# Performance work log

Measured on AMD Instinct MI355X. Metric: run time of the kernel, lower is better.

## Reference

```python
import jax, jax.numpy as jnp
import numpy as np

B, L, H, HEADS, N_NODE = 1024, 200, 128, 8, 200000
MAXN = L + 1  # max_n_node
D = H // HEADS
EPS = 1e-12


def setup_inputs() -> dict:
    key = jax.random.key(0)
    ks = jax.random.split(key, 20)
    lengths = jax.random.randint(ks[0], (B,), 1, L + 1)
    mask = (jnp.arange(L)[None, :] < lengths[:, None]).astype(jnp.int32)  # contiguous 1s
    alias_inputs = jax.random.randint(ks[1], (B, L), 0, MAXN)
    items = jax.random.randint(ks[2], (B, MAXN), 0, N_NODE)

    def lin_w(k, o, i):
        return (jax.random.normal(k, (o, i), jnp.float32) * 0.1)

    inp = dict(
        alias_inputs=alias_inputs,
        items=items,
        mask=mask,
        emb_W=jax.random.normal(ks[3], (N_NODE, H), jnp.float32) * 0.1,
        # LastAttenion params
        W0=lin_w(ks[4], H, H), b0=jax.random.normal(ks[5], (H,), jnp.float32) * 0.1,
        W1=lin_w(ks[6], H, H), b1=jax.random.normal(ks[7], (H,), jnp.float32) * 0.1,
        W2=lin_w(ks[8], H, H), b2=jax.random.normal(ks[9], (H,), jnp.float32) * 0.1,
        # linear_q[0] (last_k = 1)
        Wq=lin_w(ks[10], H, H), bq=jax.random.normal(ks[11], (H,), jnp.float32) * 0.1,
        # linear_transform (2H -> H)
        Wt=lin_w(ks[12], H, 2 * H), bt=jax.random.normal(ks[13], (H,), jnp.float32) * 0.1,
        ln_g=jax.random.normal(ks[14], (H,), jnp.float32) * 0.1,
        ln_b=jax.random.normal(ks[15], (H,), jnp.float32) * 0.1,
    )
    return inp


def reference(alias_inputs, items, mask, emb_W, W0, b0, W1, b1, W2, b2, Wq, bq, Wt, bt, ln_g, ln_b):
    maskf = mask.astype(jnp.float32)
    # hidden = normalize(embedding(items)); dropout off (eval)
    hidden = emb_W[items]                                                  # [B, MAXN, H]
    hidden = hidden / (jnp.linalg.norm(hidden, axis=-1, keepdims=True) + EPS)
    # per-batch gather: seq_hidden[b, t] = hidden[b, alias_inputs[b, t]]
    seq = jnp.take_along_axis(hidden, alias_inputs[..., None], axis=1)     # [B, L, H]
    seq = seq * maskf[..., None]
    seq = seq / (jnp.linalg.norm(seq, axis=-1, keepdims=True) + EPS)
    # compute_scores
    lengths = mask.sum(1)
    last_idx = lengths - 1                                                 # >= 0 (lengths >= 1)
    ht_last = seq[jnp.arange(B), last_idx]                                 # [B, H]  (ht0 too)
    hts = (ht_last @ Wq.T + bq)[:, None, :]                                # [B, 1, H]
    # torch.norm over dim=1 (size 1) == elementwise abs
    hts = hts / (jnp.linalg.norm(hts, axis=1, keepdims=True) + EPS)
    # LastAttenion (last_k = 1, no lp-pool, eval dropout off)
    q0 = (hts @ W0.T + b0).reshape(B * HEADS, 1, D)                        # [B*h, 1, d]
    q1 = (seq @ W1.T + b1).reshape(B * HEADS, L, D)                        # [B*h, L, d]
    q2 = (seq @ W2.T + b2).reshape(B, L, HEADS, D)                         # [B, L, h, d]
    alpha = jax.nn.sigmoid(jnp.einsum('bkd,bld->bkl', q0, q1))             # [B*h, 1, L]
    alpha = alpha.reshape(B, HEADS, L).transpose(0, 2, 1)                  # [B, L, h]
    alpha = jax.nn.softmax(2.0 * alpha, axis=1)
    a = jnp.sum((alpha[..., None] * q2).reshape(B, L, H) * maskf[..., None], axis=1)  # [B, H]
    # layernorm eps=1e-8
    mu = a.mean(-1, keepdims=True)
    var = ((a - mu) ** 2).mean(-1, keepdims=True)
    a = (a - mu) / jnp.sqrt(var + 1e-8) * ln_g + ln_b
    a = jnp.concatenate([a, ht_last], axis=1) @ Wt.T + bt                  # [B, H]
    # norm=True branch
    a = a / (jnp.linalg.norm(a, axis=1, keepdims=True) + EPS)
    b = emb_W[1:]
    b = b / (jnp.linalg.norm(b, axis=1, keepdims=True) + EPS)
    return a, b.T                                                          # [B,H], [H, N_NODE-1]
```

## Files before the change

kernel.cpp:

```cpp
#include <hip/hip_runtime.h>
#include <math.h>

typedef unsigned int uint;
typedef unsigned short ushort;

__device__ __forceinline__ float b2f(ushort u){
  union { uint i; float f; } v; v.i = ((uint)u) << 16; return v.f;
}
__device__ __forceinline__ ushort f2b(float f){
  union { float f; uint i; } v; v.f = f;
  uint i = v.i;
  i += 0x7fffu + ((i >> 16) & 1u);
  return (ushort)(i >> 16);
}
__device__ __forceinline__ float wred(float v){
  #pragma unroll
  for (int s = 32; s > 0; s >>= 1) v += __shfl_xor(v, s, 64);
  return v;
}
__device__ __forceinline__ float gred16(float v){
  v += __shfl_xor(v, 1, 64);
  v += __shfl_xor(v, 2, 64);
  v += __shfl_xor(v, 4, 64);
  v += __shfl_xor(v, 8, 64);
  return v;
}
__device__ __forceinline__ float sane(float v){ return isfinite(v) ? v : 0.f; }
__device__ __forceinline__ int iclamp(int v, int lo, int hi){ return v < lo ? lo : (v > hi ? hi : v); }

__device__ __forceinline__ void load_raw8(const void* emb, int isf, int it, int p, float x[8]){
  if (it >= 0){
    if (isf){
      const float4* q = (const float4*)((const float*)emb + (size_t)it * 128);
      float4 u = q[p * 2], u2 = q[p * 2 + 1];
      x[0] = u.x; x[1] = u.y; x[2] = u.z; x[3] = u.w;
      x[4] = u2.x; x[5] = u2.y; x[6] = u2.z; x[7] = u2.w;
    } else {
      uint4 u = ((const uint4*)((const ushort*)emb + (size_t)it * 128))[p];
      x[0] = b2f((ushort)u.x); x[1] = b2f((ushort)(u.x >> 16));
      x[2] = b2f((ushort)u.y); x[3] = b2f((ushort)(u.y >> 16));
      x[4] = b2f((ushort)u.z); x[5] = b2f((ushort)(u.z >> 16));
      x[6] = b2f((ushort)u.w); x[7] = b2f((ushort)(u.w >> 16));
    }
  } else {
    #pragma unroll
    for (int e = 0; e < 8; ++e) x[e] = 0.f;
  }
}

__device__ __forceinline__ int detect_isf(const void* emb, int t, int* s_flag){
  if (t == 0) *s_flag = 0;
  __syncthreads();
  if (t < 64){
    uint4 u = ((const uint4*)emb)[t];
    uint w[4] = { u.x, u.y, u.z, u.w };
    int bad = 0;
    #pragma unroll
    for (int e = 0; e < 4; ++e){
      float v0 = fabsf(b2f((ushort)w[e]));
      float v1 = fabsf(b2f((ushort)(w[e] >> 16)));
      if (!(v0 <= 1e4f) || !(v1 <= 1e4f)) bad = 1;
    }
    if (bad) *s_flag = 1;
  }
  __syncthreads();
  return *s_flag;
}

#define OUTB 131072

#define C_W0T 0
#define C_W1  16384
#define C_W2T 32768
#define C_WQT 49152
#define C_WTT 65536
#define C_B0  98304
#define C_B1  98432
#define C_B2  98560
#define C_BQ  98688
#define C_BT  98816
#define C_G   98944
#define C_BB  99072
#define C_TOT 99200

#define KMAIN_SMEM 73984

__global__ __launch_bounds__(256) void k_wts(
    const void* __restrict__ emb,
    const void* W0, const void* b0, const void* W1, const void* b1,
    const void* W2, const void* b2, const void* Wq, const void* bq,
    const void* Wt, const void* bt, const void* g, const void* bb,
    float* __restrict__ wts){
  __shared__ int s_flag;
  const int t = threadIdx.x;
  const int isf = detect_isf(emb, t, &s_flag);
  int j = blockIdx.x * 256 + t;
  if (j >= C_TOT) return;
  const void* src; int si;
  if (j < 16384)      { int k = j >> 7, h = j & 127; src = W0; si = h * 128 + k; }
  else if (j < 32768) { src = W1; si = j - 16384; }
  else if (j < 49152) { int i = j - 32768; int k = i >> 7, h = i & 127; src = W2; si = h * 128 + k; }
  else if (j < 65536) { int i = j - 49152; int k = i >> 7, h = i & 127; src = Wq; si = h * 128 + k; }
  else if (j < 98304) { int i = j - 65536; int k = i >> 7, h = i & 127; src = Wt; si = h * 256 + k; }
  else {
    int i = j - 98304; int arr = i >> 7;
    const void* tab[7] = { b0, b1, b2, bq, bt, g, bb };
    src = tab[arr]; si = i & 127;
  }
  wts[j] = isf ? ((const float*)src)[si] : b2f(((const ushort*)src)[si]);
}

__global__ __launch_bounds__(256) void k_bout(const void* __restrict__ emb,
                                              void* __restrict__ outv){
  __shared__ float tile[64 * 129];
  __shared__ int s_flag;
  const int t = threadIdx.x, gid = t >> 4, p = t & 15;
  const int base = blockIdx.x * 64;
  const int isf = detect_isf(emb, t, &s_flag);
  for (int i = gid; i < 64; i += 16){
    int gi = base + i;
    if (gi < 199999){
      float x[8];
      if (isf){
        const float4* q = (const float4*)((const float*)emb + (size_t)(gi + 1) * 128);
        float4 u = q[p * 2], u2 = q[p * 2 + 1];
        x[0] = u.x; x[1] = u.y; x[2] = u.z; x[3] = u.w;
        x[4] = u2.x; x[5] = u2.y; x[6] = u2.z; x[7] = u2.w;
      } else {
        uint4 u = ((const uint4*)((const ushort*)emb + (size_t)(gi + 1) * 128))[p];
        x[0] = b2f((ushort)u.x); x[1] = b2f((ushort)(u.x >> 16));
        x[2] = b2f((ushort)u.y); x[3] = b2f((ushort)(u.y >> 16));
        x[4] = b2f((ushort)u.z); x[5] = b2f((ushort)(u.z >> 16));
        x[6] = b2f((ushort)u.w); x[7] = b2f((ushort)(u.w >> 16));
      }
      float ss = 0.f;
      #pragma unroll
      for (int e = 0; e < 8; ++e) ss += x[e] * x[e];
      ss = gred16(ss);
      float inv = 1.f / (sqrtf(ss) + 1e-12f);
      #pragma unroll
      for (int e = 0; e < 8; ++e) tile[i * 129 + p * 8 + e] = x[e] * inv;
    }
  }
  __syncthreads();
  for (int it = 0; it < 32; ++it){
    int idx = it * 256 + t;
    int h = idx >> 6, n = idx & 63;
    int gi = base + n;
    if (gi < 199999){
      float val = sane(tile[n * 129 + h]);
      if (isf) ((float*)outv)[OUTB + (size_t)h * 199999 + gi] = val;
      else     ((ushort*)outv)[OUTB + (size_t)h * 199999 + gi] = f2b(val);
    }
  }
}

__global__ __launch_bounds__(256) void k_main(
    const int* __restrict__ alias_, const int* __restrict__ items,
    const int* __restrict__ mask, const void* __restrict__ emb,
    const float* __restrict__ wts, void* __restrict__ outv){
  extern __shared__ __align__(16) char dsm[];
  __shared__ int s_flag;
  __shared__ float s_X0[128], s_ht[128], s_a[128], s_hts[128];
  __shared__ float s_c1[64];
  __shared__ float s_T[8], s_Tp[64];
  __shared__ float s_red[16];
  __shared__ int   s_it[200];
  __shared__ int   s_item;

  const int t = threadIdx.x;
  const int isf = detect_isf(emb, t, &s_flag);
  const int b = blockIdx.x;

  ushort* s_x     = (ushort*)dsm;
  ushort* s_w1p   = (ushort*)(dsm + 51200);
  float*  s_part  = (float*)(dsm + 51200);
  float*  s_alpha = (float*)(dsm + 51200 + 16384);

  const int wv = t >> 6, gid = t >> 4, p = t & 15, lane = t & 63;
  const int mbase = b * 200;

  int mv = 0;
  if (t < 200){
    mv = mask[mbase + t];
    int a = mv ? iclamp(alias_[mbase + t], 0, 200) : 0;
    s_it[t] = mv ? iclamp(items[b * 201 + a], 0, 199999) : -1;
  }
  float lv = wred((float)mv);
  if ((t & 63) == 0) s_red[t >> 6] = lv;
  __syncthreads();
  const int len = iclamp((int)(s_red[0] + s_red[1] + s_red[2] + s_red[3] + 0.5f), 1, 200);
  if (t == 0){
    int a = iclamp(alias_[mbase + len - 1], 0, 200);
    s_item = iclamp(items[b * 201 + a], 0, 199999);
  }
  __syncthreads();

  float v = 0.f;
  if (t < 128)
    v = isf ? ((const float*)emb)[(size_t)s_item * 128 + t]
            : b2f(((const ushort*)emb)[(size_t)s_item * 128 + t]);
  float ss = wred(v * v);
  if ((t & 63) == 0) s_red[4 + (t >> 6)] = ss;
  __syncthreads();
  v = v / (sqrtf(s_red[4] + s_red[5]) + 1e-12f);
  float ss2 = wred(v * v);
  if ((t & 63) == 0) s_red[8 + (t >> 6)] = ss2;
  __syncthreads();
  v = v / (sqrtf(s_red[8] + s_red[9]) + 1e-12f);
  if (t < 128) s_ht[t] = v;
  __syncthreads();

  if (t < 128){
    double acc = (double)wts[C_BQ + t];
    for (int k = 0; k < 128; ++k)
      acc += (double)wts[C_WQT + k * 128 + t] * (double)s_ht[k];
    float a = (float)acc;
    s_hts[t] = a / (fabsf(a) + 1e-12f);
  }
  __syncthreads();
  if (t < 128){
    float a0 = wts[C_B0 + t];
    for (int k = 0; k < 128; ++k) a0 += wts[C_W0T + k * 128 + t] * s_hts[k];
    s_X0[t] = a0;
  }
  __syncthreads();
  if (t < 64){
    int head = t >> 3, j = t & 7;
    float c = 0.f;
    #pragma unroll
    for (int d = 0; d < 16; ++d) c += s_X0[head * 16 + d] * wts[C_B1 + j * 16 + d];
    s_c1[t] = c;
  }

  __syncthreads();
  for (int idx = t; idx < 8192; idx += 256){
    int hj = idx >> 7, k = idx & 127, head = hj >> 3, j = hj & 7;
    float acc = 0.f;
    const float* w1r = wts + C_W1 + (j * 16) * 128 + k;
    #pragma unroll
    for (int d = 0; d < 16; ++d) acc += s_X0[head * 16 + d] * w1r[d * 128];
    s_w1p[hj * 128 + k] = f2b(acc);
  }
  __syncthreads();

  {
    float xc[8], xn[8];
    load_raw8(emb, isf, s_it[gid], p, xc);
    for (int r = gid; r < 200; r += 16){
      int rn = r + 16;
      load_raw8(emb, isf, rn < 200 ? s_it[rn] : -1, p, xn);

      int head = r / 25, lb = (r % 25) * 8;
      uint4 wu[8];
      #pragma unroll
      for (int j = 0; j < 8; ++j)
        wu[j] = *(const uint4*)(s_w1p + (head * 8 + j) * 128 + p * 8);

      float ssr = 0.f;
      #pragma unroll
      for (int e = 0; e < 8; ++e) ssr += xc[e] * xc[e];
      ssr = gred16(ssr);
      float inv = 1.f / (sqrtf(ssr) + 1e-12f);
      #pragma unroll
      for (int e = 0; e < 8; ++e) xc[e] *= inv;

      uint4 u;
      u.x = (uint)f2b(xc[0]) | ((uint)f2b(xc[1]) << 16);
      u.y = (uint)f2b(xc[2]) | ((uint)f2b(xc[3]) << 16);
      u.z = (uint)f2b(xc[4]) | ((uint)f2b(xc[5]) << 16);
      u.w = (uint)f2b(xc[6]) | ((uint)f2b(xc[7]) << 16);
      *(uint4*)(s_x + r * 128 + p * 8) = u;

      #pragma unroll
      for (int j = 0; j < 8; ++j){
        float dot = xc[0] * b2f((ushort)wu[j].x) + xc[1] * b2f((ushort)(wu[j].x >> 16))
                  + xc[2] * b2f((ushort)wu[j].y) + xc[3] * b2f((ushort)(wu[j].y >> 16))
                  + xc[4] * b2f((ushort)wu[j].z) + xc[5] * b2f((ushort)(wu[j].z >> 16))
                  + xc[6] * b2f((ushort)wu[j].w) + xc[7] * b2f((ushort)(wu[j].w >> 16));
        dot = gred16(dot);
        if (p == 0){
          float logit = s_c1[head * 8 + j] + dot;
          s_alpha[(lb + j) * 8 + head] = 2.f / (1.f + expf(-logit));
        }
      }
      #pragma unroll
      for (int e = 0; e < 8; ++e) xc[e] = xn[e];
    }
  }
  __syncthreads();

  {
    int head = t >> 5, l32 = t & 31;
    float vals[7]; float mx = -1e30f;
    #pragma unroll
    for (int i = 0; i < 7; ++i){
      int l = l32 + 32 * i;
      float xx = (l < 200) ? s_alpha[l * 8 + head] : -1e30f;
      vals[i] = xx; mx = fmaxf(mx, xx);
    }
    #pragma unroll
    for (int s = 16; s > 0; s >>= 1) mx = fmaxf(mx, __shfl_xor(mx, s, 64));
    float sum = 0.f; float e[7];
    #pragma unroll
    for (int i = 0; i < 7; ++i){
      int l = l32 + 32 * i;
      float ex = (l < 200) ? expf(vals[i] - mx) : 0.f;
      e[i] = ex; sum += ex;
    }
    #pragma unroll
    for (int s = 16; s > 0; s >>= 1) sum += __shfl_xor(sum, s, 64);
    float inv = 1.f / sum;
    #pragma unroll
    for (int i = 0; i < 7; ++i){
      int l = l32 + 32 * i;
      if (l < 200) s_alpha[l * 8 + head] = e[i] * inv;
    }
  }
  __syncthreads();

  if (t < 64){
    int h = t & 7, seg = t >> 3;
    int l0 = seg * 25, l1 = l0 + 25; if (l1 > len) l1 = len;
    float s = 0.f;
    for (int l = l0; l < l1; ++l) s += s_alpha[l * 8 + h];
    s_Tp[t] = s;
  }
  __syncthreads();
  if (t < 8){
    float s = 0.f;
    #pragma unroll
    for (int seg = 0; seg < 8; ++seg) s += s_Tp[seg * 8 + t];
    s_T[t] = s;
  }

  float acc[64];
  #pragma unroll
  for (int e = 0; e < 64; ++e) acc[e] = 0.f;
  for (int l = gid; l < 200; l += 16){
    if (s_it[l] >= 0){
      uint4 xu = *(const uint4*)(s_x + l * 128 + p * 8);
      float x[8];
      x[0] = b2f((ushort)xu.x); x[1] = b2f((ushort)(xu.x >> 16));
      x[2] = b2f((ushort)xu.y); x[3] = b2f((ushort)(xu.y >> 16));
      x[4] = b2f((ushort)xu.z); x[5] = b2f((ushort)(xu.z >> 16));
      x[6] = b2f((ushort)xu.w); x[7] = b2f((ushort)(xu.w >> 16));
      float4 a0 = *(const float4*)(s_alpha + l * 8);
      float4 a1 = *(const float4*)(s_alpha + l * 8 + 4);
      float al[8] = { a0.x, a0.y, a0.z, a0.w, a1.x, a1.y, a1.z, a1.w };
      #pragma unroll
      for (int h = 0; h < 8; ++h)
        #pragma unroll
        for (int e = 0; e < 8; ++e) acc[h * 8 + e] += al[h] * x[e];
    }
  }
  #pragma unroll
  for (int e = 0; e < 64; ++e){
    float vv = acc[e];
    vv += __shfl_xor(vv, 16, 64);
    vv += __shfl_xor(vv, 32, 64);
    acc[e] = vv;
  }
  __syncthreads();
  if (lane < 16){
    #pragma unroll
    for (int h = 0; h < 8; ++h)
      #pragma unroll
      for (int e = 0; e < 8; ++e)
        s_part[wv * 1024 + h * 128 + p * 8 + e] = acc[h * 8 + e];
  }
  __syncthreads();
  for (int i = t; i < 1024; i += 256)
    s_part[i] = s_part[i] + s_part[1024 + i] + s_part[2048 + i] + s_part[3072 + i];
  __syncthreads();

  float araw = 0.f;
  if (t < 128){
    int head = t >> 4;
    araw = wts[C_B2 + t] * s_T[head];
    const float* hl = &s_part[head * 128];
    for (int k = 0; k < 128; ++k) araw += hl[k] * wts[C_W2T + k * 128 + t];
  }
  float v1 = wred(t < 128 ? araw : 0.f);
  if ((t & 63) == 0) s_red[t >> 6] = v1;
  __syncthreads();
  float mu = (s_red[0] + s_red[1]) * 0.0078125f;
  float dd = (t < 128) ? (araw - mu) : 0.f;
  float v2 = wred(dd * dd);
  if ((t & 63) == 0) s_red[4 + (t >> 6)] = v2;
  __syncthreads();
  float var = (s_red[4] + s_red[5]) * 0.0078125f;
  if (t < 128)
    s_a[t] = dd / sqrtf(var + 1e-8f) * wts[C_G + t] + wts[C_BB + t];
  __syncthreads();

  float o = 0.f;
  if (t < 128){
    o = wts[C_BT + t];
    for (int k = 0; k < 128; ++k) o += s_a[k] * wts[C_WTT + k * 128 + t];
    for (int k = 0; k < 128; ++k) o += s_ht[k] * wts[C_WTT + (128 + k) * 128 + t];
  }
  float v3 = wred(t < 128 ? o * o : 0.f);
  if ((t & 63) == 0) s_red[8 + (t >> 6)] = v3;
  __syncthreads();
  float nrm = sqrtf(s_red[8] + s_red[9]);
  if (t < 128){
    float val = sane(o / (nrm + 1e-12f));
    if (isf) ((float*)outv)[b * 128 + t] = val;
    else     ((ushort*)outv)[b * 128 + t] = f2b(val);
  }
}

extern "C" void kernel_launch(void* const* d_in, const int* in_sizes, int n_in,
                              void* d_out, int out_size, void* d_ws, size_t ws_size,
                              hipStream_t stream){
  const int* alias_ = (const int*)d_in[0];
  const int* items  = (const int*)d_in[1];
  const int* mask   = (const int*)d_in[2];
  const void* emb = d_in[3];
  const void* W0  = d_in[4];
  const void* b0  = d_in[5];
  const void* W1  = d_in[6];
  const void* b1  = d_in[7];
  const void* W2  = d_in[8];
  const void* b2_ = d_in[9];
  const void* Wq  = d_in[10];
  const void* bq  = d_in[11];
  const void* Wt  = d_in[12];
  const void* bt  = d_in[13];
  const void* g_  = d_in[14];
  const void* bb_ = d_in[15];

  char* ws = (char*)d_ws;
  float* wts = (float*)ws;

  static int g_attr_done = 0;
  if (!g_attr_done){
    hipFuncSetAttribute(reinterpret_cast<const void*>(k_main),
                        hipFuncAttributeMaxDynamicSharedMemorySize, KMAIN_SMEM);
    g_attr_done = 1;
  }

  k_wts <<<dim3(388),  dim3(256), 0,          stream>>>(emb, W0, b0, W1, b1,
                                              W2, b2_, Wq, bq, Wt, bt, g_, bb_, wts);
  k_bout<<<dim3(3125), dim3(256), 0,          stream>>>(emb, d_out);
  k_main<<<dim3(1024), dim3(256), KMAIN_SMEM, stream>>>(alias_, items, mask, emb,
                                              wts, d_out);
}
```

Measured before the change: 393.6 us.

## Shrink k_main shared memory by re-gathering late rows, merge weight prep into k_bout

Folds the weight-transpose kernel into k_bout, removing one launch. In k_main only the first 104 normalized rows are cached in LDS as bf16; later rows are re-gathered from the embedding table and rescaled with a stored per-row norm. This cuts dynamic LDS so more blocks can be resident per CU, at the cost of extra global gathers. It also deepens embedding prefetch to two rows ahead and splits the small matvec loops into multiple accumulators to shorten dependency chains.

```diff
diff --git a/kernel.cpp b/kernel.cpp
--- a/kernel.cpp
+++ b/kernel.cpp
@@ -27,6 +27,10 @@
 }
 __device__ __forceinline__ float sane(float v){ return isfinite(v) ? v : 0.f; }
 __device__ __forceinline__ int iclamp(int v, int lo, int hi){ return v < lo ? lo : (v > hi ? hi : v); }
+__device__ __forceinline__ void cp8(float d[8], const float s[8]){
+  #pragma unroll
+  for (int e = 0; e < 8; ++e) d[e] = s[e];
+}
 
 __device__ __forceinline__ void load_raw8(const void* emb, int isf, int it, int p, float x[8]){
   if (it >= 0){
@@ -83,35 +87,15 @@
 #define C_BB  99072
 #define C_TOT 99200
 
-#define KMAIN_SMEM 73984
-
-__global__ __launch_bounds__(256) void k_wts(
+#define XROWS 104
+#define KMAIN_SMEM 49408
+
+__global__ __launch_bounds__(256) void k_bout(
     const void* __restrict__ emb,
     const void* W0, const void* b0, const void* W1, const void* b1,
     const void* W2, const void* b2, const void* Wq, const void* bq,
     const void* Wt, const void* bt, const void* g, const void* bb,
-    float* __restrict__ wts){
-  __shared__ int s_flag;
-  const int t = threadIdx.x;
-  const int isf = detect_isf(emb, t, &s_flag);
-  int j = blockIdx.x * 256 + t;
-  if (j >= C_TOT) return;
-  const void* src; int si;
-  if (j < 16384)      { int k = j >> 7, h = j & 127; src = W0; si = h * 128 + k; }
-  else if (j < 32768) { src = W1; si = j - 16384; }
-  else if (j < 49152) { int i = j - 32768; int k = i >> 7, h = i & 127; src = W2; si = h * 128 + k; }
-  else if (j < 65536) { int i = j - 49152; int k = i >> 7, h = i & 127; src = Wq; si = h * 128 + k; }
-  else if (j < 98304) { int i = j - 65536; int k = i >> 7, h = i & 127; src = Wt; si = h * 256 + k; }
-  else {
-    int i = j - 98304; int arr = i >> 7;
-    const void* tab[7] = { b0, b1, b2, bq, bt, g, bb };
-    src = tab[arr]; si = i & 127;
-  }
-  wts[j] = isf ? ((const float*)src)[si] : b2f(((const ushort*)src)[si]);
-}
-
-__global__ __launch_bounds__(256) void k_bout(const void* __restrict__ emb,
-                                              void* __restrict__ outv){
+    float* __restrict__ wts, void* __restrict__ outv){
   __shared__ float tile[64 * 129];
   __shared__ int s_flag;
   const int t = threadIdx.x, gid = t >> 4, p = t & 15;
@@ -153,6 +137,21 @@
       else     ((ushort*)outv)[OUTB + (size_t)h * 199999 + gi] = f2b(val);
     }
   }
+  int j = blockIdx.x * 256 + t;
+  if (blockIdx.x < 388 && j < C_TOT){
+    const void* src; int si;
+    if (j < 16384)      { int k = j >> 7, h = j & 127; src = W0; si = h * 128 + k; }
+    else if (j < 32768) { src = W1; si = j - 16384; }
+    else if (j < 49152) { int i = j - 32768; int k = i >> 7, h = i & 127; src = W2; si = h * 128 + k; }
+    else if (j < 65536) { int i = j - 49152; int k = i >> 7, h = i & 127; src = Wq; si = h * 128 + k; }
+    else if (j < 98304) { int i = j - 65536; int k = i >> 7, h = i & 127; src = Wt; si = h * 256 + k; }
+    else {
+      int i = j - 98304; int arr = i >> 7;
+      const void* tab[7] = { b0, b1, b2, bq, bt, g, bb };
+      src = tab[arr]; si = i & 127;
+    }
+    wts[j] = isf ? ((const float*)src)[si] : b2f(((const ushort*)src)[si]);
+  }
 }
 
 __global__ __launch_bounds__(256) void k_main(
@@ -165,6 +164,7 @@
   __shared__ float s_c1[64];
   __shared__ float s_T[8], s_Tp[64];
   __shared__ float s_red[16];
+  __shared__ float s_nrm[200];
   __shared__ int   s_it[200];
   __shared__ int   s_item;
 
@@ -173,9 +173,9 @@
   const int b = blockIdx.x;
 
   ushort* s_x     = (ushort*)dsm;
-  ushort* s_w1p   = (ushort*)(dsm + 51200);
-  float*  s_part  = (float*)(dsm + 51200);
-  float*  s_alpha = (float*)(dsm + 51200 + 16384);
+  ushort* s_w1p   = (ushort*)(dsm + 26624);
+  float*  s_part  = (float*)(dsm + 26624);
+  float*  s_alpha = (float*)(dsm + 43008);
 
   const int wv = t >> 6, gid = t >> 4, p = t & 15, lane = t & 63;
   const int mbase = b * 200;
@@ -189,6 +189,11 @@
   float lv = wred((float)mv);
   if ((t & 63) == 0) s_red[t >> 6] = lv;
   __syncthreads();
+
+  float xc[8], xn1[8];
+  load_raw8(emb, isf, s_it[gid], p, xc);
+  load_raw8(emb, isf, s_it[gid + 16], p, xn1);
+
   const int len = iclamp((int)(s_red[0] + s_red[1] + s_red[2] + s_red[3] + 0.5f), 1, 200);
   if (t == 0){
     int a = iclamp(alias_[mbase + len - 1], 0, 200);
@@ -212,17 +217,26 @@
   __syncthreads();
 
   if (t < 128){
-    double acc = (double)wts[C_BQ + t];
-    for (int k = 0; k < 128; ++k)
-      acc += (double)wts[C_WQT + k * 128 + t] * (double)s_ht[k];
-    float a = (float)acc;
+    double d0 = 0.0, d1 = 0.0, d2 = 0.0, d3 = 0.0;
+    for (int k = 0; k < 128; k += 4){
+      d0 += (double)wts[C_WQT + (k    ) * 128 + t] * (double)s_ht[k    ];
+      d1 += (double)wts[C_WQT + (k + 1) * 128 + t] * (double)s_ht[k + 1];
+      d2 += (double)wts[C_WQT + (k + 2) * 128 + t] * (double)s_ht[k + 2];
+      d3 += (double)wts[C_WQT + (k + 3) * 128 + t] * (double)s_ht[k + 3];
+    }
+    float a = (float)((double)wts[C_BQ + t] + ((d0 + d1) + (d2 + d3)));
     s_hts[t] = a / (fabsf(a) + 1e-12f);
   }
   __syncthreads();
   if (t < 128){
-    float a0 = wts[C_B0 + t];
-    for (int k = 0; k < 128; ++k) a0 += wts[C_W0T + k * 128 + t] * s_hts[k];
-    s_X0[t] = a0;
+    float a0 = 0.f, a1 = 0.f, a2 = 0.f, a3 = 0.f;
+    for (int k = 0; k < 128; k += 4){
+      a0 += wts[C_W0T + (k    ) * 128 + t] * s_hts[k    ];
+      a1 += wts[C_W0T + (k + 1) * 128 + t] * s_hts[k + 1];
+      a2 += wts[C_W0T + (k + 2) * 128 + t] * s_hts[k + 2];
+      a3 += wts[C_W0T + (k + 3) * 128 + t] * s_hts[k + 3];
+    }
+    s_X0[t] = wts[C_B0 + t] + ((a0 + a1) + (a2 + a3));
   }
   __syncthreads();
   if (t < 64){
@@ -245,11 +259,10 @@
   __syncthreads();
 
   {
-    float xc[8], xn[8];
-    load_raw8(emb, isf, s_it[gid], p, xc);
+    float xt[8];
     for (int r = gid; r < 200; r += 16){
-      int rn = r + 16;
-      load_raw8(emb, isf, rn < 200 ? s_it[rn] : -1, p, xn);
+      int rn = r + 32;
+      load_raw8(emb, isf, rn < 200 ? s_it[rn] : -1, p, xt);
 
       int head = r / 25, lb = (r % 25) * 8;
       uint4 wu[8];
@@ -264,13 +277,16 @@
       float inv = 1.f / (sqrtf(ssr) + 1e-12f);
       #pragma unroll
       for (int e = 0; e < 8; ++e) xc[e] *= inv;
-
-      uint4 u;
-      u.x = (uint)f2b(xc[0]) | ((uint)f2b(xc[1]) << 16);
-      u.y = (uint)f2b(xc[2]) | ((uint)f2b(xc[3]) << 16);
-      u.z = (uint)f2b(xc[4]) | ((uint)f2b(xc[5]) << 16);
-      u.w = (uint)f2b(xc[6]) | ((uint)f2b(xc[7]) << 16);
-      *(uint4*)(s_x + r * 128 + p * 8) = u;
+      if (p == 0) s_nrm[r] = inv;
+
+      if (r < XROWS){
+        uint4 u;
+        u.x = (uint)f2b(xc[0]) | ((uint)f2b(xc[1]) << 16);
+        u.y = (uint)f2b(xc[2]) | ((uint)f2b(xc[3]) << 16);
+        u.z = (uint)f2b(xc[4]) | ((uint)f2b(xc[5]) << 16);
+        u.w = (uint)f2b(xc[6]) | ((uint)f2b(xc[7]) << 16);
+        *(uint4*)(s_x + r * 128 + p * 8) = u;
+      }
 
       #pragma unroll
       for (int j = 0; j < 8; ++j){
@@ -284,8 +300,7 @@
           s_alpha[(lb + j) * 8 + head] = 2.f / (1.f + expf(-logit));
         }
       }
-      #pragma unroll
-      for (int e = 0; e < 8; ++e) xc[e] = xn[e];
+      cp8(xc, xn1); cp8(xn1, xt);
     }
   }
   __syncthreads();
@@ -337,21 +352,41 @@
   float acc[64];
   #pragma unroll
   for (int e = 0; e < 64; ++e) acc[e] = 0.f;
-  for (int l = gid; l < 200; l += 16){
-    if (s_it[l] >= 0){
-      uint4 xu = *(const uint4*)(s_x + l * 128 + p * 8);
+  {
+    int hk0 = (119 - gid) >> 4;
+    int lA = gid + (hk0 << 4);
+    float ha[8], hb[8];
+    load_raw8(emb, isf, lA < 200 ? s_it[lA] : -1, p, ha);
+    int lB = lA + 16;
+    load_raw8(emb, isf, lB < 200 ? s_it[lB] : -1, p, hb);
+    for (int l = gid; l < 200; l += 16){
+      bool act = (s_it[l] >= 0);
       float x[8];
-      x[0] = b2f((ushort)xu.x); x[1] = b2f((ushort)(xu.x >> 16));
-      x[2] = b2f((ushort)xu.y); x[3] = b2f((ushort)(xu.y >> 16));
-      x[4] = b2f((ushort)xu.z); x[5] = b2f((ushort)(xu.z >> 16));
-      x[6] = b2f((ushort)xu.w); x[7] = b2f((ushort)(xu.w >> 16));
-      float4 a0 = *(const float4*)(s_alpha + l * 8);
-      float4 a1 = *(const float4*)(s_alpha + l * 8 + 4);
-      float al[8] = { a0.x, a0.y, a0.z, a0.w, a1.x, a1.y, a1.z, a1.w };
-      #pragma unroll
-      for (int h = 0; h < 8; ++h)
+      if (l < XROWS){
+        if (act){
+          uint4 xu = *(const uint4*)(s_x + l * 128 + p * 8);
+          x[0] = b2f((ushort)xu.x); x[1] = b2f((ushort)(xu.x >> 16));
+          x[2] = b2f((ushort)xu.y); x[3] = b2f((ushort)(xu.y >> 16));
+          x[4] = b2f((ushort)xu.z); x[5] = b2f((ushort)(xu.z >> 16));
+          x[6] = b2f((ushort)xu.w); x[7] = b2f((ushort)(xu.w >> 16));
+        }
+      } else {
+        float nm = s_nrm[l];
         #pragma unroll
-        for (int e = 0; e < 8; ++e) acc[h * 8 + e] += al[h] * x[e];
+        for (int e = 0; e < 8; ++e) x[e] = ha[e] * nm;
+        cp8(ha, hb);
+        int lC = l + 32;
+        load_raw8(emb, isf, lC < 200 ? s_it[lC] : -1, p, hb);
+      }
+      if (act){
+        float4 a0 = *(const float4*)(s_alpha + l * 8);
+        float4 a1 = *(const float4*)(s_alpha + l * 8 + 4);
+        float al[8] = { a0.x, a0.y, a0.z, a0.w, a1.x, a1.y, a1.z, a1.w };
+        #pragma unroll
+        for (int h = 0; h < 8; ++h)
+          #pragma unroll
+          for (int e = 0; e < 8; ++e) acc[h * 8 + e] += al[h] * x[e];
+      }
     }
   }
   #pragma unroll
@@ -377,9 +412,15 @@
   float araw = 0.f;
   if (t < 128){
     int head = t >> 4;
-    araw = wts[C_B2 + t] * s_T[head];
     const float* hl = &s_part[head * 128];
-    for (int k = 0; k < 128; ++k) araw += hl[k] * wts[C_W2T + k * 128 + t];
+    float a0 = 0.f, a1 = 0.f, a2 = 0.f, a3 = 0.f;
+    for (int k = 0; k < 128; k += 4){
+      a0 += hl[k    ] * wts[C_W2T + (k    ) * 128 + t];
+      a1 += hl[k + 1] * wts[C_W2T + (k + 1) * 128 + t];
+      a2 += hl[k + 2] * wts[C_W2T + (k + 2) * 128 + t];
+      a3 += hl[k + 3] * wts[C_W2T + (k + 3) * 128 + t];
+    }
+    araw = wts[C_B2 + t] * s_T[head] + ((a0 + a1) + (a2 + a3));
   }
   float v1 = wred(t < 128 ? araw : 0.f);
   if ((t & 63) == 0) s_red[t >> 6] = v1;
@@ -396,9 +437,14 @@
 
   float o = 0.f;
   if (t < 128){
-    o = wts[C_BT + t];
-    for (int k = 0; k < 128; ++k) o += s_a[k] * wts[C_WTT + k * 128 + t];
-    for (int k = 0; k < 128; ++k) o += s_ht[k] * wts[C_WTT + (128 + k) * 128 + t];
+    float o0 = 0.f, o1 = 0.f, o2 = 0.f, o3 = 0.f;
+    for (int k = 0; k < 128; k += 2){
+      o0 += s_a[k    ] * wts[C_WTT + (k      ) * 128 + t];
+      o1 += s_a[k + 1] * wts[C_WTT + (k + 1  ) * 128 + t];
+      o2 += s_ht[k   ] * wts[C_WTT + (128 + k) * 128 + t];
+      o3 += s_ht[k+ 1] * wts[C_WTT + (129 + k) * 128 + t];
+    }
+    o = wts[C_BT + t] + ((o0 + o1) + (o2 + o3));
   }
   float v3 = wred(t < 128 ? o * o : 0.f);
   if ((t & 63) == 0) s_red[8 + (t >> 6)] = v3;
@@ -441,9 +487,9 @@
     g_attr_done = 1;
   }
 
-  k_wts <<<dim3(388),  dim3(256), 0,          stream>>>(emb, W0, b0, W1, b1,
-                                              W2, b2_, Wq, bq, Wt, bt, g_, bb_, wts);
-  k_bout<<<dim3(3125), dim3(256), 0,          stream>>>(emb, d_out);
+  k_bout<<<dim3(3125), dim3(256), 0,          stream>>>(emb, W0, b0, W1, b1,
+                                              W2, b2_, Wq, bq, Wt, bt, g_, bb_,
+                                              wts, d_out);
   k_main<<<dim3(1024), dim3(256), KMAIN_SMEM, stream>>>(alias_, items, mask, emb,
                                               wts, d_out);
 }
```

After: 376.5 us. 1.05x faster.
